# Kernel optimization log

Hardware: AMD Instinct MI355X
Metric: run time of the kernel (lower is better)

The kernel has to match this reference:

```python
import jax, jax.numpy as jnp
import numpy as np

# dims
B, S = 1, 32768          # batch, grid seqlen (32^3 latent grid)
NQ, NE = 32768, 262144   # mesh query nodes, grid->query edges
IN, EMB, HID, BOT, PREDH, OUT, NDIM = 192, 192, 192, 192, 192, 4, 3
MAX_WAVELENGTH = 10000.0


def sincos_embed(coords, dim, ndim):
    # ContinuousSincosEmbed: dim % ndim == 0 and (dim//ndim) even here -> no padding
    eff = dim // ndim                                     # 64 dims per coordinate
    omega = 1.0 / MAX_WAVELENGTH ** (jnp.arange(0, eff, 2, dtype=jnp.float32) / eff)  # [eff//2]
    out = coords[..., None] * omega                       # [N, ndim, eff//2]
    emb = jnp.concatenate([jnp.sin(out), jnp.cos(out)], axis=-1)  # [N, ndim, eff]
    return emb.reshape(coords.shape[0], ndim * eff)       # [N, dim]


def _linear_params(key, fan_in, fan_out):
    k1, k2 = jax.random.split(key)
    lim = 1.0 / np.sqrt(fan_in)
    w = jax.random.uniform(k1, (fan_in, fan_out), jnp.float32, -lim, lim)
    b = jax.random.uniform(k2, (fan_out,), jnp.float32, -lim, lim)
    return w, b


def setup_inputs() -> dict:
    key = jax.random.key(0)
    ks = jax.random.split(key, 10)
    x = jax.random.normal(ks[0], (B, S, IN), jnp.float32)
    query_pos = jax.random.uniform(ks[1], (NQ, NDIM), jnp.float32) * 100.0
    # edges sorted by query index (required by the CSR segment reduce in the original)
    qidx = jnp.sort(jax.random.randint(ks[2], (NE,), 0, NQ))
    gidx = jax.random.randint(ks[3], (NE,), 0, B * S)
    grid_to_query_edges = jnp.stack([qidx, gidx], axis=1).astype(jnp.int64)
    proj_w, proj_b = _linear_params(ks[4], IN, EMB)
    msg0_w, msg0_b = _linear_params(ks[5], 2 * EMB, 2 * HID)
    msg1_w, msg1_b = _linear_params(ks[6], 2 * HID, 2 * HID)
    msg2_w, msg2_b = _linear_params(ks[7], 2 * HID, BOT)
    pred0_w, pred0_b = _linear_params(ks[8], BOT, PREDH)
    pred1_w, pred1_b = _linear_params(ks[9], PREDH, OUT)
    return dict(x=x, query_pos=query_pos, grid_to_query_edges=grid_to_query_edges,
                proj_w=proj_w, proj_b=proj_b,
                msg0_w=msg0_w, msg0_b=msg0_b, msg1_w=msg1_w, msg1_b=msg1_b,
                msg2_w=msg2_w, msg2_b=msg2_b,
                pred0_w=pred0_w, pred0_b=pred0_b, pred1_w=pred1_w, pred1_b=pred1_b)


def reference(x, query_pos, grid_to_query_edges,
              proj_w, proj_b, msg0_w, msg0_b, msg1_w, msg1_b, msg2_w, msg2_b,
              pred0_w, pred0_b, pred1_w, pred1_b):
    gelu = lambda t: jax.nn.gelu(t, approximate=False)  # torch nn.GELU default (erf)
    # flatten grid tokens and project
    xf = x.reshape(-1, x.shape[-1]) @ proj_w + proj_b          # [B*S, EMB]
    qe = sincos_embed(query_pos, EMB, NDIM)                    # [NQ, EMB]
    qidx = grid_to_query_edges[:, 0]
    gidx = grid_to_query_edges[:, 1]
    # gather + concat per edge
    h = jnp.concatenate([xf[gidx], qe[qidx]], axis=1)          # [NE, 2*EMB]
    # message MLP
    h = gelu(h @ msg0_w + msg0_b)
    h = gelu(h @ msg1_w + msg1_b)
    h = h @ msg2_w + msg2_b                                    # [NE, BOT]
    # segment mean to query nodes (empty segments -> 0, matching segment_csr mean)
    nq = query_pos.shape[0]
    seg_sum = jax.ops.segment_sum(h, qidx, num_segments=nq)    # [NQ, BOT]
    cnt = jax.ops.segment_sum(jnp.ones((qidx.shape[0], 1), h.dtype), qidx, num_segments=nq)
    m = seg_sum / jnp.maximum(cnt, 1.0)
    # prediction head
    out = gelu(m @ pred0_w + pred0_b) @ pred1_w + pred1_b      # [NQ, OUT]
    return out
```

## Files before the change

kernel.cpp:

```cpp
#include <hip/hip_runtime.h>
#include <math.h>

#define N_Q    32768
#define N_E    262144

typedef _Float16 half8 __attribute__((ext_vector_type(8)));
typedef _Float16 half4v __attribute__((ext_vector_type(4)));
typedef float f32x4 __attribute__((ext_vector_type(4)));

__device__ __forceinline__ float gelu_f(float x) {
    float ax = fabsf(x);
    float t = __builtin_amdgcn_rcpf(fmaf(0.33269070724668f, ax, 1.0f));
    float poly = t * fmaf(t, fmaf(t, 0.7478556f, -0.0958798f), 0.3480242f);
    float e = exp2f(-0.72134752044448f * ax * ax);
    float u = fmaf(-poly, e, 1.0f);
    return 0.5f * fmaf(ax, u, x);
}

__global__ __launch_bounds__(256) void embed_kernel(const float* __restrict__ qpos,
                                                    _Float16* __restrict__ qe) {
    int gid = blockIdx.x * 256 + threadIdx.x;
    int q = gid / 96, r = gid - q * 96;
    int d = r >> 5, i = r & 31;
    float omega = exp2f(-(float)i * 0.41524101186092029f);
    float arg = qpos[q * 3 + d] * omega;
    float rev = arg * 0.15915494309189535f;
    rev = rev - floorf(rev);
    float s = __builtin_amdgcn_sinf(rev);
    float c = __builtin_amdgcn_cosf(rev);
    int base = q * 192 + d * 64 + i;
    qe[base] = (_Float16)s;
    qe[base + 32] = (_Float16)c;
}

__device__ __forceinline__ void pack_one(const float* __restrict__ W,
                                         _Float16* __restrict__ Wp,
                                         int K, int N, int blk0, int tid) {
    int u = blk0 * 256 + tid;
    if (u * 8 >= K * N) return;
    int l = u & 63, blk = u >> 6;
    int nks = K >> 5;
    int ntile = blk / nks, ks = blk - ntile * nks;
    int n = ntile * 16 + (l & 15);
    int k0 = ks * 32 + (l >> 4) * 8;
    half8 v;
    #pragma unroll
    for (int j = 0; j < 8; ++j) v[j] = (_Float16)W[(size_t)(k0 + j) * N + n];
    *(half8*)(Wp + (size_t)u * 8) = v;
}

__global__ __launch_bounds__(256) void pack_all_kernel(
    const float* __restrict__ pw,  _Float16* __restrict__ WpP,
    const float* __restrict__ m0,  _Float16* __restrict__ Wp0,
    const float* __restrict__ m1,  _Float16* __restrict__ Wp1,
    const float* __restrict__ m2,  _Float16* __restrict__ Wp2,
    const float* __restrict__ hw,  _Float16* __restrict__ WpH) {
    int b = blockIdx.x, t = threadIdx.x;
    if      (b < 18)  pack_one(pw, WpP, 192, 192, b,        t);
    else if (b < 90)  pack_one(m0, Wp0, 384, 384, b - 18,   t);
    else if (b < 162) pack_one(m1, Wp1, 384, 384, b - 90,   t);
    else if (b < 198) pack_one(m2, Wp2, 384, 192, b - 162,  t);
    else              pack_one(hw, WpH, 192, 192, b - 198,  t);
}

#define PK 200

__global__ __launch_bounds__(256, 2) void proj_mfma_kernel(
    const float* __restrict__ x, const _Float16* __restrict__ Wp,
    const float* __restrict__ bias, _Float16* __restrict__ xf)
{
    __shared__ _Float16 hA[64 * PK];
    const int t = threadIdx.x;
    const int r0 = blockIdx.x * 64;
    const int lane = t & 63;
    const int w = t >> 6;
    const int ln = lane & 15, lq = lane >> 4;

    #pragma unroll
    for (int i = 0; i < 12; ++i) {
        int idx = t + 256 * i;
        int r = idx / 48, c4 = idx - r * 48;
        float4 v = ((const float4*)(x + (size_t)(r0 + r) * 192))[c4];
        half4v hv; hv[0] = (_Float16)v.x; hv[1] = (_Float16)v.y;
        hv[2] = (_Float16)v.z; hv[3] = (_Float16)v.w;
        *(half4v*)(hA + r * PK + c4 * 4) = hv;
    }
    __syncthreads();

    f32x4 acc[4][3];
    #pragma unroll
    for (int nt = 0; nt < 3; ++nt) {
        f32x4 bv = *(const f32x4*)(bias + w * 48 + nt * 16 + lq * 4);
        #pragma unroll
        for (int mt = 0; mt < 4; ++mt) acc[mt][nt] = bv;
    }
    #pragma unroll 2
    for (int ks = 0; ks < 6; ++ks) {
        half8 a[4], bf[3];
        #pragma unroll
        for (int mt = 0; mt < 4; ++mt)
            a[mt] = *(const half8*)(hA + (mt * 16 + ln) * PK + ks * 32 + lq * 8);
        #pragma unroll
        for (int nt = 0; nt < 3; ++nt)
            bf[nt] = *(const half8*)(Wp + (size_t)(((w * 3 + nt) * 6 + ks) * 512 + lane * 8));
        #pragma unroll
        for (int nt = 0; nt < 3; ++nt)
            #pragma unroll
            for (int mt = 0; mt < 4; ++mt)
                acc[mt][nt] = __builtin_amdgcn_mfma_f32_16x16x32_f16(bf[nt], a[mt], acc[mt][nt], 0, 0, 0);
    }
    #pragma unroll
    for (int mt = 0; mt < 4; ++mt)
        #pragma unroll
        for (int nt = 0; nt < 3; ++nt) {
            half4v hv;
            #pragma unroll
            for (int r = 0; r < 4; ++r) hv[r] = (_Float16)acc[mt][nt][r];
            *(half4v*)(xf + (size_t)(r0 + mt * 16 + ln) * 192 + w * 48 + nt * 16 + lq * 4) = hv;
        }
}

#define PADK 392
#define H2S  196

__global__ __launch_bounds__(512, 6) void edge_mlp_kernel(
    const _Float16* __restrict__ xf, const _Float16* __restrict__ qe,
    const int* __restrict__ edges,
    const _Float16* __restrict__ Wp0, const float* __restrict__ b0,
    const _Float16* __restrict__ Wp1, const float* __restrict__ b1,
    const _Float16* __restrict__ Wp2, const float* __restrict__ b2,
    float* __restrict__ seg, float* __restrict__ cnt)
{
    __shared__ _Float16 hA[64 * PADK];
    __shared__ int qi[64];
    float* h2 = (float*)hA;

    const int t = threadIdx.x;
    const int e0 = blockIdx.x * 64;
    const int lane = t & 63;
    const int w = t >> 6;
    const int ln = lane & 15;
    const int lq = lane >> 4;

    if (t < 64) qi[t] = edges[2 * (e0 + t)];

    {
        const int m = t >> 3;
        const int cl = t & 7;
        int2 eg = ((const int2*)edges)[e0 + m];
        const half8* xsrc = (const half8*)(xf + (size_t)eg.y * 192) + cl;
        const half8* qsrc = (const half8*)(qe + (size_t)eg.x * 192) + cl;
        half8* dst = (half8*)(hA + m * PADK + cl * 8);
        #pragma unroll
        for (int i = 0; i < 3; ++i) dst[i * 8] = xsrc[i * 8];
        #pragma unroll
        for (int i = 0; i < 3; ++i) dst[24 + i * 8] = qsrc[i * 8];
    }
    __syncthreads();

    #pragma unroll 1
    for (int L = 0; L < 2; ++L) {
        const _Float16* __restrict__ Wp = L ? Wp1 : Wp0;
        const float* __restrict__ bias = L ? b1 : b0;

        f32x4 acc[4][3];
        #pragma unroll
        for (int nt = 0; nt < 3; ++nt) {
            f32x4 bv = *(const f32x4*)(bias + w * 48 + nt * 16 + lq * 4);
            #pragma unroll
            for (int mt = 0; mt < 4; ++mt) acc[mt][nt] = bv;
        }
        #pragma unroll 2
        for (int ks = 0; ks < 12; ++ks) {
            half8 a[4], bf[3];
            #pragma unroll
            for (int mt = 0; mt < 4; ++mt)
                a[mt] = *(const half8*)(hA + (mt * 16 + ln) * PADK + ks * 32 + lq * 8);
            #pragma unroll
            for (int nt = 0; nt < 3; ++nt)
                bf[nt] = *(const half8*)(Wp + (size_t)(((w * 3 + nt) * 12 + ks) * 512 + lane * 8));
            #pragma unroll
            for (int nt = 0; nt < 3; ++nt)
                #pragma unroll
                for (int mt = 0; mt < 4; ++mt)
                    acc[mt][nt] = __builtin_amdgcn_mfma_f32_16x16x32_f16(bf[nt], a[mt], acc[mt][nt], 0, 0, 0);
        }
        __syncthreads();
        #pragma unroll
        for (int mt = 0; mt < 4; ++mt)
            #pragma unroll
            for (int nt = 0; nt < 3; ++nt) {
                half4v hv;
                #pragma unroll
                for (int r = 0; r < 4; ++r) hv[r] = (_Float16)gelu_f(acc[mt][nt][r]);
                *(half4v*)(hA + (mt * 16 + ln) * PADK + w * 48 + nt * 16 + lq * 4) = hv;
            }
        __syncthreads();
    }

    {
        const int n0 = (w & 3) * 48;
        const int mh = (w >> 2) * 2;
        f32x4 acc[2][3];
        #pragma unroll
        for (int nt = 0; nt < 3; ++nt) {
            f32x4 bv = *(const f32x4*)(b2 + n0 + nt * 16 + lq * 4);
            #pragma unroll
            for (int mt = 0; mt < 2; ++mt) acc[mt][nt] = bv;
        }
        #pragma unroll 2
        for (int ks = 0; ks < 12; ++ks) {
            half8 a[2], bf[3];
            #pragma unroll
            for (int mt = 0; mt < 2; ++mt)
                a[mt] = *(const half8*)(hA + ((mh + mt) * 16 + ln) * PADK + ks * 32 + lq * 8);
            #pragma unroll
            for (int nt = 0; nt < 3; ++nt)
                bf[nt] = *(const half8*)(Wp2 + (size_t)((((w & 3) * 3 + nt) * 12 + ks) * 512 + lane * 8));
            #pragma unroll
            for (int nt = 0; nt < 3; ++nt)
                #pragma unroll
                for (int mt = 0; mt < 2; ++mt)
                    acc[mt][nt] = __builtin_amdgcn_mfma_f32_16x16x32_f16(bf[nt], a[mt], acc[mt][nt], 0, 0, 0);
        }
        __syncthreads();
        #pragma unroll
        for (int mt = 0; mt < 2; ++mt)
            #pragma unroll
            for (int nt = 0; nt < 3; ++nt)
                *(f32x4*)(h2 + ((mh + mt) * 16 + ln) * H2S + n0 + nt * 16 + lq * 4) = acc[mt][nt];
        __syncthreads();
    }

    if (t < 384) {
        int half_ = t >= 192;
        int col = t - half_ * 192;
        int mlo = half_ * 32, mhi = mlo + 32;
        float a = 0.0f;
        for (int m = mlo; m < mhi; ++m) {
            a += h2[m * H2S + col];
            if (m == mhi - 1 || qi[m + 1] != qi[m]) {
                atomicAdd(&seg[(size_t)qi[m] * 192 + col], a);
                a = 0.0f;
            }
        }
    } else if (t < 386) {
        int half_ = t - 384;
        int mlo = half_ * 32, mhi = mlo + 32;
        float run = 1.0f;
        for (int m = mlo + 1; m < mhi; ++m) {
            if (qi[m] != qi[m - 1]) { atomicAdd(&cnt[qi[m - 1]], run); run = 1.0f; }
            else run += 1.0f;
        }
        atomicAdd(&cnt[qi[mhi - 1]], run);
    }
}

#define PSK 196

__global__ __launch_bounds__(256, 2) void head_kernel(
    const float* __restrict__ seg, const float* __restrict__ cnt,
    const _Float16* __restrict__ Wp0, const float* __restrict__ b0,
    const float* __restrict__ w1, const float* __restrict__ b1,
    float* __restrict__ out)
{
    __shared__ _Float16 hA[64 * PK];
    __shared__ float ps[64 * PSK];
    __shared__ float w1s[192 * 4];
    __shared__ float invc[64];
    const int t = threadIdx.x;
    const int r0 = blockIdx.x * 64;
    const int lane = t & 63;
    const int w = t >> 6;
    const int ln = lane & 15, lq = lane >> 4;

    if (t < 64) invc[t] = 1.0f / fmaxf(cnt[r0 + t], 1.0f);
    if (t < 192) ((float4*)w1s)[t] = ((const float4*)w1)[t];
    __syncthreads();

    #pragma unroll
    for (int i = 0; i < 12; ++i) {
        int idx = t + 256 * i;
        int r = idx / 48, c4 = idx - r * 48;
        float inv = invc[r];
        float4 v = ((const float4*)(seg + (size_t)(r0 + r) * 192))[c4];
        half4v hv; hv[0] = (_Float16)(v.x * inv); hv[1] = (_Float16)(v.y * inv);
        hv[2] = (_Float16)(v.z * inv); hv[3] = (_Float16)(v.w * inv);
        *(half4v*)(hA + r * PK + c4 * 4) = hv;
    }
    __syncthreads();

    f32x4 acc[4][3];
    #pragma unroll
    for (int nt = 0; nt < 3; ++nt) {
        f32x4 bv = *(const f32x4*)(b0 + w * 48 + nt * 16 + lq * 4);
        #pragma unroll
        for (int mt = 0; mt < 4; ++mt) acc[mt][nt] = bv;
    }
    #pragma unroll 2
    for (int ks = 0; ks < 6; ++ks) {
        half8 a[4], bf[3];
        #pragma unroll
        for (int mt = 0; mt < 4; ++mt)
            a[mt] = *(const half8*)(hA + (mt * 16 + ln) * PK + ks * 32 + lq * 8);
        #pragma unroll
        for (int nt = 0; nt < 3; ++nt)
            bf[nt] = *(const half8*)(Wp0 + (size_t)(((w * 3 + nt) * 6 + ks) * 512 + lane * 8));
        #pragma unroll
        for (int nt = 0; nt < 3; ++nt)
            #pragma unroll
            for (int mt = 0; mt < 4; ++mt)
                acc[mt][nt] = __builtin_amdgcn_mfma_f32_16x16x32_f16(bf[nt], a[mt], acc[mt][nt], 0, 0, 0);
    }
    #pragma unroll
    for (int mt = 0; mt < 4; ++mt)
        #pragma unroll
        for (int nt = 0; nt < 3; ++nt) {
            f32x4 g;
            #pragma unroll
            for (int r = 0; r < 4; ++r) g[r] = gelu_f(acc[mt][nt][r]);
            *(f32x4*)(ps + (mt * 16 + ln) * PSK + w * 48 + nt * 16 + lq * 4) = g;
        }
    __syncthreads();

    {
        int r = t >> 2, oo = t & 3;
        float a = b1[oo];
        for (int k = 0; k < 192; ++k)
            a = fmaf(ps[r * PSK + k], w1s[k * 4 + oo], a);
        out[(size_t)(r0 + r) * 4 + oo] = a;
    }
}

extern "C" void kernel_launch(void* const* d_in, const int* in_sizes, int n_in,
                              void* d_out, int out_size, void* d_ws, size_t ws_size,
                              hipStream_t stream) {
    (void)in_sizes; (void)n_in; (void)out_size; (void)ws_size;
    const float* x       = (const float*)d_in[0];
    const float* qpos    = (const float*)d_in[1];
    const int*   edges   = (const int*)d_in[2];
    const float* proj_w  = (const float*)d_in[3];
    const float* proj_b  = (const float*)d_in[4];
    const float* msg0_w  = (const float*)d_in[5];
    const float* msg0_b  = (const float*)d_in[6];
    const float* msg1_w  = (const float*)d_in[7];
    const float* msg1_b  = (const float*)d_in[8];
    const float* msg2_w  = (const float*)d_in[9];
    const float* msg2_b  = (const float*)d_in[10];
    const float* pred0_w = (const float*)d_in[11];
    const float* pred0_b = (const float*)d_in[12];
    const float* pred1_w = (const float*)d_in[13];
    const float* pred1_b = (const float*)d_in[14];
    float* out = (float*)d_out;

    char* ws = (char*)d_ws;
    _Float16* xf  = (_Float16*)(ws);
    _Float16* qe  = (_Float16*)(ws + 12582912);
    float*    seg = (float*)(ws + 25165824);
    float*    cnt = (float*)(ws + 50331648);
    _Float16* Wp0 = (_Float16*)(ws + 50462720);
    _Float16* Wp1 = (_Float16*)(ws + 50757632);
    _Float16* Wp2 = (_Float16*)(ws + 51052544);
    _Float16* WpP = (_Float16*)(ws + 51200000);
    _Float16* WpH = (_Float16*)(ws + 51273728);

    hipMemsetAsync(seg, 0, 25165824 + 131072, stream);
    embed_kernel<<<12288, 256, 0, stream>>>(qpos, qe);
    pack_all_kernel<<<216, 256, 0, stream>>>(proj_w, WpP, msg0_w, Wp0,
                                             msg1_w, Wp1, msg2_w, Wp2,
                                             pred0_w, WpH);
    proj_mfma_kernel<<<512, 256, 0, stream>>>(x, WpP, proj_b, xf);
    edge_mlp_kernel<<<4096, 512, 0, stream>>>(xf, qe, edges,
                                              Wp0, msg0_b, Wp1, msg1_b, Wp2, msg2_b,
                                              seg, cnt);
    head_kernel<<<512, 256, 0, stream>>>(seg, cnt, WpH, pred0_b,
                                         pred1_w, pred1_b, out);
}
```

Baseline: 384.0 us.

## Split first message layer into per-node precomputed projections gathered per edge

```diff
diff --git a/kernel.cpp b/kernel.cpp
--- a/kernel.cpp
+++ b/kernel.cpp
@@ -17,20 +17,25 @@
     return 0.5f * fmaf(ax, u, x);
 }
 
-__global__ __launch_bounds__(256) void embed_kernel(const float* __restrict__ qpos,
-                                                    _Float16* __restrict__ qe) {
+__global__ __launch_bounds__(256) void prep_kernel(
+    const float* __restrict__ proj_w, const float* __restrict__ proj_b,
+    const float* __restrict__ msg0_w, const float* __restrict__ msg0_b,
+    float* __restrict__ Wc, float* __restrict__ bc)
+{
     int gid = blockIdx.x * 256 + threadIdx.x;
-    int q = gid / 96, r = gid - q * 96;
-    int d = r >> 5, i = r & 31;
-    float omega = exp2f(-(float)i * 0.41524101186092029f);
-    float arg = qpos[q * 3 + d] * omega;
-    float rev = arg * 0.15915494309189535f;
-    rev = rev - floorf(rev);
-    float s = __builtin_amdgcn_sinf(rev);
-    float c = __builtin_amdgcn_cosf(rev);
-    int base = q * 192 + d * 64 + i;
-    qe[base] = (_Float16)s;
-    qe[base + 32] = (_Float16)c;
+    if (gid < 73728) {
+        int j = gid / 384, n = gid - j * 384;
+        float a = 0.0f;
+        for (int k = 0; k < 192; ++k)
+            a = fmaf(proj_w[j * 192 + k], msg0_w[k * 384 + n], a);
+        Wc[gid] = a;
+    } else if (gid < 73728 + 384) {
+        int n = gid - 73728;
+        float a = msg0_b[n];
+        for (int k = 0; k < 192; ++k)
+            a = fmaf(proj_b[k], msg0_w[k * 384 + n], a);
+        bc[n] = a;
+    }
 }
 
 __device__ __forceinline__ void pack_one(const float* __restrict__ W,
@@ -50,24 +55,24 @@
 }
 
 __global__ __launch_bounds__(256) void pack_all_kernel(
-    const float* __restrict__ pw,  _Float16* __restrict__ WpP,
-    const float* __restrict__ m0,  _Float16* __restrict__ Wp0,
+    const float* __restrict__ Wc,  _Float16* __restrict__ WpC,
+    const float* __restrict__ m0,  _Float16* __restrict__ WpQ,
     const float* __restrict__ m1,  _Float16* __restrict__ Wp1,
     const float* __restrict__ m2,  _Float16* __restrict__ Wp2,
     const float* __restrict__ hw,  _Float16* __restrict__ WpH) {
     int b = blockIdx.x, t = threadIdx.x;
-    if      (b < 18)  pack_one(pw, WpP, 192, 192, b,        t);
-    else if (b < 90)  pack_one(m0, Wp0, 384, 384, b - 18,   t);
-    else if (b < 162) pack_one(m1, Wp1, 384, 384, b - 90,   t);
-    else if (b < 198) pack_one(m2, Wp2, 384, 192, b - 162,  t);
-    else              pack_one(hw, WpH, 192, 192, b - 198,  t);
+    if      (b < 36)  pack_one(Wc,          WpC, 192, 384, b,       t);
+    else if (b < 72)  pack_one(m0 + 73728,  WpQ, 192, 384, b - 36,  t);
+    else if (b < 144) pack_one(m1,          Wp1, 384, 384, b - 72,  t);
+    else if (b < 180) pack_one(m2,          Wp2, 384, 192, b - 144, t);
+    else              pack_one(hw,          WpH, 192, 192, b - 180, t);
 }
 
 #define PK 200
 
-__global__ __launch_bounds__(256, 2) void proj_mfma_kernel(
-    const float* __restrict__ x, const _Float16* __restrict__ Wp,
-    const float* __restrict__ bias, _Float16* __restrict__ xf)
+__global__ __launch_bounds__(256, 2) void pg_kernel(
+    const float* __restrict__ x, const _Float16* __restrict__ WpC,
+    const float* __restrict__ bc, _Float16* __restrict__ pg)
 {
     __shared__ _Float16 hA[64 * PK];
     const int t = threadIdx.x;
@@ -87,24 +92,24 @@
     }
     __syncthreads();
 
-    f32x4 acc[4][3];
-    #pragma unroll
-    for (int nt = 0; nt < 3; ++nt) {
-        f32x4 bv = *(const f32x4*)(bias + w * 48 + nt * 16 + lq * 4);
+    f32x4 acc[4][6];
+    #pragma unroll
+    for (int nt = 0; nt < 6; ++nt) {
+        f32x4 bv = *(const f32x4*)(bc + w * 96 + nt * 16 + lq * 4);
         #pragma unroll
         for (int mt = 0; mt < 4; ++mt) acc[mt][nt] = bv;
     }
     #pragma unroll 2
     for (int ks = 0; ks < 6; ++ks) {
-        half8 a[4], bf[3];
+        half8 a[4], bf[6];
         #pragma unroll
         for (int mt = 0; mt < 4; ++mt)
             a[mt] = *(const half8*)(hA + (mt * 16 + ln) * PK + ks * 32 + lq * 8);
         #pragma unroll
-        for (int nt = 0; nt < 3; ++nt)
-            bf[nt] = *(const half8*)(Wp + (size_t)(((w * 3 + nt) * 6 + ks) * 512 + lane * 8));
-        #pragma unroll
-        for (int nt = 0; nt < 3; ++nt)
+        for (int nt = 0; nt < 6; ++nt)
+            bf[nt] = *(const half8*)(WpC + (size_t)(((w * 6 + nt) * 6 + ks) * 512 + lane * 8));
+        #pragma unroll
+        for (int nt = 0; nt < 6; ++nt)
             #pragma unroll
             for (int mt = 0; mt < 4; ++mt)
                 acc[mt][nt] = __builtin_amdgcn_mfma_f32_16x16x32_f16(bf[nt], a[mt], acc[mt][nt], 0, 0, 0);
@@ -112,11 +117,67 @@
     #pragma unroll
     for (int mt = 0; mt < 4; ++mt)
         #pragma unroll
-        for (int nt = 0; nt < 3; ++nt) {
+        for (int nt = 0; nt < 6; ++nt) {
             half4v hv;
             #pragma unroll
             for (int r = 0; r < 4; ++r) hv[r] = (_Float16)acc[mt][nt][r];
-            *(half4v*)(xf + (size_t)(r0 + mt * 16 + ln) * 192 + w * 48 + nt * 16 + lq * 4) = hv;
+            *(half4v*)(pg + (size_t)(r0 + mt * 16 + ln) * 384 + w * 96 + nt * 16 + lq * 4) = hv;
+        }
+}
+
+__global__ __launch_bounds__(256, 2) void pq_kernel(
+    const float* __restrict__ qpos, const _Float16* __restrict__ WpQ,
+    _Float16* __restrict__ pq)
+{
+    __shared__ _Float16 hA[64 * PK];
+    const int t = threadIdx.x;
+    const int r0 = blockIdx.x * 64;
+    const int lane = t & 63;
+    const int w = t >> 6;
+    const int ln = lane & 15, lq = lane >> 4;
+
+    #pragma unroll
+    for (int it = 0; it < 24; ++it) {
+        int g2 = t + 256 * it;
+        int r = g2 / 96, rem = g2 - r * 96;
+        int d = rem >> 5, i = rem & 31;
+        float omega = exp2f(-(float)i * 0.41524101186092029f);
+        float arg = qpos[(size_t)(r0 + r) * 3 + d] * omega;
+        float rev = arg * 0.15915494309189535f;
+        rev = rev - floorf(rev);
+        hA[r * PK + d * 64 + i]      = (_Float16)__builtin_amdgcn_sinf(rev);
+        hA[r * PK + d * 64 + 32 + i] = (_Float16)__builtin_amdgcn_cosf(rev);
+    }
+    __syncthreads();
+
+    f32x4 acc[4][6];
+    #pragma unroll
+    for (int nt = 0; nt < 6; ++nt)
+        #pragma unroll
+        for (int mt = 0; mt < 4; ++mt) acc[mt][nt] = (f32x4){0.f, 0.f, 0.f, 0.f};
+    #pragma unroll 2
+    for (int ks = 0; ks < 6; ++ks) {
+        half8 a[4], bf[6];
+        #pragma unroll
+        for (int mt = 0; mt < 4; ++mt)
+            a[mt] = *(const half8*)(hA + (mt * 16 + ln) * PK + ks * 32 + lq * 8);
+        #pragma unroll
+        for (int nt = 0; nt < 6; ++nt)
+            bf[nt] = *(const half8*)(WpQ + (size_t)(((w * 6 + nt) * 6 + ks) * 512 + lane * 8));
+        #pragma unroll
+        for (int nt = 0; nt < 6; ++nt)
+            #pragma unroll
+            for (int mt = 0; mt < 4; ++mt)
+                acc[mt][nt] = __builtin_amdgcn_mfma_f32_16x16x32_f16(bf[nt], a[mt], acc[mt][nt], 0, 0, 0);
+    }
+    #pragma unroll
+    for (int mt = 0; mt < 4; ++mt)
+        #pragma unroll
+        for (int nt = 0; nt < 6; ++nt) {
+            half4v hv;
+            #pragma unroll
+            for (int r = 0; r < 4; ++r) hv[r] = (_Float16)acc[mt][nt][r];
+            *(half4v*)(pq + (size_t)(r0 + mt * 16 + ln) * 384 + w * 96 + nt * 16 + lq * 4) = hv;
         }
 }
 
@@ -124,9 +185,8 @@
 #define H2S  196
 
 __global__ __launch_bounds__(512, 6) void edge_mlp_kernel(
-    const _Float16* __restrict__ xf, const _Float16* __restrict__ qe,
+    const _Float16* __restrict__ pg, const _Float16* __restrict__ pq,
     const int* __restrict__ edges,
-    const _Float16* __restrict__ Wp0, const float* __restrict__ b0,
     const _Float16* __restrict__ Wp1, const float* __restrict__ b1,
     const _Float16* __restrict__ Wp2, const float* __restrict__ b2,
     float* __restrict__ seg, float* __restrict__ cnt)
@@ -148,25 +208,27 @@
         const int m = t >> 3;
         const int cl = t & 7;
         int2 eg = ((const int2*)edges)[e0 + m];
-        const half8* xsrc = (const half8*)(xf + (size_t)eg.y * 192) + cl;
-        const half8* qsrc = (const half8*)(qe + (size_t)eg.x * 192) + cl;
+        const half8* gsrc = (const half8*)(pg + (size_t)eg.y * 384) + cl;
+        const half8* qsrc = (const half8*)(pq + (size_t)eg.x * 384) + cl;
         half8* dst = (half8*)(hA + m * PADK + cl * 8);
         #pragma unroll
-        for (int i = 0; i < 3; ++i) dst[i * 8] = xsrc[i * 8];
-        #pragma unroll
-        for (int i = 0; i < 3; ++i) dst[24 + i * 8] = qsrc[i * 8];
-    }
-    __syncthreads();
-
-    #pragma unroll 1
-    for (int L = 0; L < 2; ++L) {
-        const _Float16* __restrict__ Wp = L ? Wp1 : Wp0;
-        const float* __restrict__ bias = L ? b1 : b0;
-
+        for (int i = 0; i < 6; ++i) {
+            half8 va = gsrc[i * 8];
+            half8 vb = qsrc[i * 8];
+            half8 o;
+            #pragma unroll
+            for (int j = 0; j < 8; ++j)
+                o[j] = (_Float16)gelu_f((float)va[j] + (float)vb[j]);
+            dst[i * 8] = o;
+        }
+    }
+    __syncthreads();
+
+    {
         f32x4 acc[4][3];
         #pragma unroll
         for (int nt = 0; nt < 3; ++nt) {
-            f32x4 bv = *(const f32x4*)(bias + w * 48 + nt * 16 + lq * 4);
+            f32x4 bv = *(const f32x4*)(b1 + w * 48 + nt * 16 + lq * 4);
             #pragma unroll
             for (int mt = 0; mt < 4; ++mt) acc[mt][nt] = bv;
         }
@@ -178,7 +240,7 @@
                 a[mt] = *(const half8*)(hA + (mt * 16 + ln) * PADK + ks * 32 + lq * 8);
             #pragma unroll
             for (int nt = 0; nt < 3; ++nt)
-                bf[nt] = *(const half8*)(Wp + (size_t)(((w * 3 + nt) * 12 + ks) * 512 + lane * 8));
+                bf[nt] = *(const half8*)(Wp1 + (size_t)(((w * 3 + nt) * 12 + ks) * 512 + lane * 8));
             #pragma unroll
             for (int nt = 0; nt < 3; ++nt)
                 #pragma unroll
@@ -354,24 +416,27 @@
     float* out = (float*)d_out;
 
     char* ws = (char*)d_ws;
-    _Float16* xf  = (_Float16*)(ws);
-    _Float16* qe  = (_Float16*)(ws + 12582912);
-    float*    seg = (float*)(ws + 25165824);
-    float*    cnt = (float*)(ws + 50331648);
-    _Float16* Wp0 = (_Float16*)(ws + 50462720);
-    _Float16* Wp1 = (_Float16*)(ws + 50757632);
-    _Float16* Wp2 = (_Float16*)(ws + 51052544);
-    _Float16* WpP = (_Float16*)(ws + 51200000);
-    _Float16* WpH = (_Float16*)(ws + 51273728);
+    _Float16* pg  = (_Float16*)(ws);
+    _Float16* pq  = (_Float16*)(ws + 25165824);
+    float*    seg = (float*)(ws + 50331648);
+    float*    cnt = (float*)(ws + 75497472);
+    float*    Wc  = (float*)(ws + 75628544);
+    float*    bc  = (float*)(ws + 75923456);
+    _Float16* WpC = (_Float16*)(ws + 75924992);
+    _Float16* WpQ = (_Float16*)(ws + 76072448);
+    _Float16* Wp1 = (_Float16*)(ws + 76219904);
+    _Float16* Wp2 = (_Float16*)(ws + 76514816);
+    _Float16* WpH = (_Float16*)(ws + 76662272);
 
     hipMemsetAsync(seg, 0, 25165824 + 131072, stream);
-    embed_kernel<<<12288, 256, 0, stream>>>(qpos, qe);
-    pack_all_kernel<<<216, 256, 0, stream>>>(proj_w, WpP, msg0_w, Wp0,
+    prep_kernel<<<290, 256, 0, stream>>>(proj_w, proj_b, msg0_w, msg0_b, Wc, bc);
+    pack_all_kernel<<<198, 256, 0, stream>>>(Wc, WpC, msg0_w, WpQ,
                                              msg1_w, Wp1, msg2_w, Wp2,
                                              pred0_w, WpH);
-    proj_mfma_kernel<<<512, 256, 0, stream>>>(x, WpP, proj_b, xf);
-    edge_mlp_kernel<<<4096, 512, 0, stream>>>(xf, qe, edges,
-                                              Wp0, msg0_b, Wp1, msg1_b, Wp2, msg2_b,
+    pg_kernel<<<512, 256, 0, stream>>>(x, WpC, bc, pg);
+    pq_kernel<<<512, 256, 0, stream>>>(qpos, WpQ, pq);
+    edge_mlp_kernel<<<4096, 512, 0, stream>>>(pg, pq, edges,
+                                              Wp1, msg1_b, Wp2, msg2_b,
                                               seg, cnt);
     head_kernel<<<512, 256, 0, stream>>>(seg, cnt, WpH, pred0_b,
                                          pred1_w, pred1_b, out);
```

Measured after the change: 345.9 us. 9.9% less time.
